# Kernel optimization log

Hardware: AMD Instinct MI355X
Metric: run time of the kernel (lower is better)

The kernel has to match this reference:

```python
import jax, jax.numpy as jnp
import numpy as np

N, D_IN, D_ATTN = 8192, 48, 8


def setup_inputs() -> dict:
    key = jax.random.key(0)
    ks = jax.random.split(key, 9)
    s = 1.0 / np.sqrt(D_IN)
    return {
        "x": jax.random.normal(ks[0], (N, D_IN), jnp.float32),
        "Kw": jax.random.normal(ks[1], (D_IN, D_ATTN), jnp.float32) * s,
        "Kb": jax.random.normal(ks[2], (D_ATTN,), jnp.float32) * s,
        "Qw": jax.random.normal(ks[3], (D_IN, D_ATTN), jnp.float32) * s,
        "Qb": jax.random.normal(ks[4], (D_ATTN,), jnp.float32) * s,
        "Vw": jax.random.normal(ks[5], (D_IN, D_ATTN), jnp.float32) * s,
        "Vb": jax.random.normal(ks[6], (D_ATTN,), jnp.float32) * s,
        "Zw": jax.random.normal(ks[7], (D_ATTN, D_IN), jnp.float32) * (1.0 / np.sqrt(D_ATTN)),
        "Zb": jax.random.normal(ks[8], (D_IN,), jnp.float32) * (1.0 / np.sqrt(D_ATTN)),
    }


def reference(x, Kw, Kb, Qw, Qb, Vw, Vb, Zw, Zb):
    # Tiny QKV projections: [N,48] -> [N,8]
    Xk = x @ Kw + Kb
    Xq = x @ Qw + Qb
    Xv = x @ Vw + Vb
    # Attention over the batch/row dimension: [N,8]@[8,N] -> [N,N]
    scale = jnp.sqrt(jnp.asarray(D_ATTN, jnp.float32))
    AM = jax.nn.softmax(Xk @ Xq.T / scale, axis=1)  # torch F.softmax 2D default dim=1
    Z = AM @ Xv                                      # [N,8]
    return x + (Z @ Zw + Zb)                         # residual + output proj [N,48]
```

## Files before the change

kernel.cpp:

```cpp
#include <hip/hip_runtime.h>
#include <hip/hip_fp16.h>


#define QVJ_OFF  32768
#define BMAX_OFF 131072
#define PART_OFF 131328

typedef _Float16 hv2 __attribute__((ext_vector_type(2)));
union HVU { unsigned u; hv2 v; };

static __device__ __forceinline__ unsigned pku(float a, float b) {
    auto t = __builtin_amdgcn_cvt_pkrtz(a, b);
    union { decltype(t) x; unsigned u; } c; c.x = t; return c.u;
}
static __device__ __forceinline__ float loF(unsigned u) { HVU t; t.u = u; return (float)t.v.x; }
static __device__ __forceinline__ float hiF(unsigned u) { HVU t; t.u = u; return (float)t.v.y; }

__global__ __launch_bounds__(256) void proj_kernel(
    const float* __restrict__ x,
    const float* __restrict__ Kw, const float* __restrict__ Kb,
    const float* __restrict__ Qw, const float* __restrict__ Qb,
    const float* __restrict__ Vw, const float* __restrict__ Vb,
    unsigned* __restrict__ Xksf16, unsigned* __restrict__ QVJ,
    float* __restrict__ bmax)
{
    __shared__ float xs[32 * 49];
    __shared__ float wAll[3 * 388];
    __shared__ float bs[24];
    __shared__ float outv[32][25];
    const int tid = threadIdx.x;
    const int r0 = blockIdx.x * 32;

    for (int i = tid; i < 1536; i += 256) {
        int r = i / 48, c = i - r * 48;
        xs[r * 49 + c] = x[r0 * 48 + i];
    }
    for (int i = tid; i < 384; i += 256) {
        wAll[i]       = Kw[i];
        wAll[388 + i] = Qw[i];
        wAll[776 + i] = Vw[i];
    }
    if (tid < 8)       bs[tid] = Kb[tid];
    else if (tid < 16) bs[tid] = Qb[tid - 8];
    else if (tid < 24) bs[tid] = Vb[tid - 16];
    __syncthreads();

    const int rl = tid >> 3;
    const int g  = tid & 7;
    const int c0 = 3 * g;
    const float* xr = &xs[rl * 49];
    const float* w0 = &wAll[((c0 + 0) >> 3) * 388 + ((c0 + 0) & 7)];
    const float* w1 = &wAll[((c0 + 1) >> 3) * 388 + ((c0 + 1) & 7)];
    const float* w2 = &wAll[((c0 + 2) >> 3) * 388 + ((c0 + 2) & 7)];
    float a0 = bs[c0], a1 = bs[c0 + 1], a2 = bs[c0 + 2];
    #pragma unroll
    for (int k = 0; k < 48; k++) {
        const float xv = xr[k];
        a0 = fmaf(xv, w0[k * 8], a0);
        a1 = fmaf(xv, w1[k * 8], a1);
        a2 = fmaf(xv, w2[k * 8], a2);
    }
    outv[rl][c0] = a0; outv[rl][c0 + 1] = a1; outv[rl][c0 + 2] = a2;
    __syncthreads();

    for (int i = tid; i < 384; i += 256) {
        const int r = i / 12, f = i - r * 12;
        unsigned val;
        if (f < 8) {
            val = __float_as_uint(outv[r][8 + f]);
        } else {
            const int pp = f - 8;
            val = pku(outv[r][16 + 2 * pp], outv[r][16 + 2 * pp + 1]);
        }
        QVJ[((size_t)blockIdx.x * 32 + r) * 12 + f] = val;
    }
    const float kscale = 0.51008732149f;
    if (tid < 32) {
        uint4 o;
        o.x = pku(outv[tid][0] * kscale, outv[tid][1] * kscale);
        o.y = pku(outv[tid][2] * kscale, outv[tid][3] * kscale);
        o.z = pku(outv[tid][4] * kscale, outv[tid][5] * kscale);
        o.w = pku(outv[tid][6] * kscale, outv[tid][7] * kscale);
        ((uint4*)Xksf16)[r0 + tid] = o;
    }
    if (tid >= 192 && tid < 224) {
        const int r = tid - 192;
        float n2 = 0.f;
        #pragma unroll
        for (int c = 0; c < 8; c++) n2 = fmaf(outv[r][8 + c], outv[r][8 + c], n2);
        #pragma unroll
        for (int off = 16; off > 0; off >>= 1)
            n2 = fmaxf(n2, __shfl_xor(n2, off, 64));
        if (r == 0) bmax[blockIdx.x] = n2;
    }
}

__global__ __launch_bounds__(256) void attn_kernel(
    const unsigned* __restrict__ Xksf16, const unsigned* __restrict__ QVJ,
    const float* __restrict__ bmax,
    float* __restrict__ part, int jpw)
{
    __shared__ float shf[4 * 256 * 9];
    uint4*  slab4 = (uint4*)shf;
    float4* slabf = (float4*)shf;
    float*  redf  = shf;

    const int tid  = threadIdx.x;
    const int lane = tid & 63;
    const int wv   = tid >> 6;
    const int rgrp  = blockIdx.x & 31;
    const int chunk = blockIdx.x >> 5;

    float m = fmaxf(fmaxf(bmax[lane], bmax[64 + lane]),
                    fmaxf(bmax[128 + lane], bmax[192 + lane]));
    #pragma unroll
    for (int off = 32; off > 0; off >>= 1)
        m = fmaxf(m, __shfl_xor(m, off, 64));
    const float qmax2 = m;

    float kf[4][8];
    float sinit[4], l[4], acc[4][8];
    #pragma unroll
    for (int i = 0; i < 4; ++i) {
        const uint4 kv = ((const uint4*)Xksf16)[rgrp * 256 + i * 64 + lane];
        kf[i][0] = loF(kv.x); kf[i][1] = hiF(kv.x);
        kf[i][2] = loF(kv.y); kf[i][3] = hiF(kv.y);
        kf[i][4] = loF(kv.z); kf[i][5] = hiF(kv.z);
        kf[i][6] = loF(kv.w); kf[i][7] = hiF(kv.w);
        float kn2 = 0.f;
        #pragma unroll
        for (int c = 0; c < 8; c++) kn2 = fmaf(kf[i][c], kf[i][c], kn2);
        sinit[i] = -sqrtf(kn2 * qmax2);
        l[i] = 0.f;
        #pragma unroll
        for (int c = 0; c < 8; c++) acc[i][c] = 0.f;
    }

    const uint4* QVJ4 = (const uint4*)QVJ;
    const int nt = jpw >> 6;

    for (int t = 0; t < nt; ++t) {
        for (int i = tid; i < 768; i += 256) {
            const int w = i / 192, rec = i - w * 192;
            slab4[i] = QVJ4[((size_t)(chunk * 4 + w) * jpw + t * 64) * 3 + rec];
        }
        __syncthreads();

        const int wbase = wv * 192;
        #pragma unroll 1
        for (int jj = 0; jj < 32; ++jj) {
            const int b = wbase + jj * 6;
            const float4 qa0 = slabf[b + 0];
            const float4 qa1 = slabf[b + 1];
            const uint4  va  = slab4[b + 2];
            const float4 qb0 = slabf[b + 3];
            const float4 qb1 = slabf[b + 4];
            const uint4  vb  = slab4[b + 5];
            const float vA0 = loF(va.x), vA1 = hiF(va.x), vA2 = loF(va.y), vA3 = hiF(va.y);
            const float vA4 = loF(va.z), vA5 = hiF(va.z), vA6 = loF(va.w), vA7 = hiF(va.w);
            const float vB0 = loF(vb.x), vB1 = hiF(vb.x), vB2 = loF(vb.y), vB3 = hiF(vb.y);
            const float vB4 = loF(vb.z), vB5 = hiF(vb.z), vB6 = loF(vb.w), vB7 = hiF(vb.w);
            #pragma unroll
            for (int i = 0; i < 4; ++i) {
                float sA = sinit[i];
                sA = fmaf(kf[i][0], qa0.x, sA);
                sA = fmaf(kf[i][1], qa0.y, sA);
                sA = fmaf(kf[i][2], qa0.z, sA);
                sA = fmaf(kf[i][3], qa0.w, sA);
                sA = fmaf(kf[i][4], qa1.x, sA);
                sA = fmaf(kf[i][5], qa1.y, sA);
                sA = fmaf(kf[i][6], qa1.z, sA);
                sA = fmaf(kf[i][7], qa1.w, sA);
                float sB = sinit[i];
                sB = fmaf(kf[i][0], qb0.x, sB);
                sB = fmaf(kf[i][1], qb0.y, sB);
                sB = fmaf(kf[i][2], qb0.z, sB);
                sB = fmaf(kf[i][3], qb0.w, sB);
                sB = fmaf(kf[i][4], qb1.x, sB);
                sB = fmaf(kf[i][5], qb1.y, sB);
                sB = fmaf(kf[i][6], qb1.z, sB);
                sB = fmaf(kf[i][7], qb1.w, sB);
                const float pA = __builtin_amdgcn_exp2f(sA);
                const float pB = __builtin_amdgcn_exp2f(sB);
                l[i] += pA + pB;
                acc[i][0] = fmaf(pA, vA0, fmaf(pB, vB0, acc[i][0]));
                acc[i][1] = fmaf(pA, vA1, fmaf(pB, vB1, acc[i][1]));
                acc[i][2] = fmaf(pA, vA2, fmaf(pB, vB2, acc[i][2]));
                acc[i][3] = fmaf(pA, vA3, fmaf(pB, vB3, acc[i][3]));
                acc[i][4] = fmaf(pA, vA4, fmaf(pB, vB4, acc[i][4]));
                acc[i][5] = fmaf(pA, vA5, fmaf(pB, vB5, acc[i][5]));
                acc[i][6] = fmaf(pA, vA6, fmaf(pB, vB6, acc[i][6]));
                acc[i][7] = fmaf(pA, vA7, fmaf(pB, vB7, acc[i][7]));
            }
        }
        __syncthreads();
    }

    #pragma unroll
    for (int i = 0; i < 4; ++i) {
        const int r = i * 64 + lane;
        #pragma unroll
        for (int c = 0; c < 8; c++)
            redf[(wv * 256 + r) * 9 + c] = acc[i][c];
        redf[(wv * 256 + r) * 9 + 8] = l[i];
    }
    __syncthreads();
    for (int e = tid; e < 2304; e += 256) {
        const int r = e / 9, c = e - r * 9;
        const float s = redf[(0 * 256 + r) * 9 + c] + redf[(1 * 256 + r) * 9 + c]
                      + redf[(2 * 256 + r) * 9 + c] + redf[(3 * 256 + r) * 9 + c];
        part[((size_t)chunk * 8192 + rgrp * 256 + r) * 9 + c] = s;
    }
}

__global__ __launch_bounds__(256) void finish_kernel(
    const float* __restrict__ x,
    const float* __restrict__ Zw, const float* __restrict__ Zb,
    const float* __restrict__ part, float* __restrict__ out, int nch)
{
    __shared__ float Zs[32 * 9];
    __shared__ float Zl[32];
    __shared__ float zw_s[384];
    __shared__ float zb_s[48];
    const int tid = threadIdx.x;
    const int r0 = blockIdx.x * 32;

    for (int i = tid; i < 384; i += 256) zw_s[i] = Zw[i];
    if (tid < 48) zb_s[tid] = Zb[tid];

    {
        const int r = tid >> 3, c = tid & 7;
        float a = 0.f, l = 0.f;
        #pragma unroll 4
        for (int ch = 0; ch < nch; ch++) {
            const float* p = part + ((size_t)ch * 8192 + r0 + r) * 9;
            a += p[c];
            if (c == 0) l += p[8];
        }
        if (c == 0) Zl[r] = l;
        __syncthreads();
        Zs[r * 9 + c] = a * (1.0f / Zl[r]);
    }
    __syncthreads();

    for (int e = tid; e < 32 * 48; e += 256) {
        const int r = e / 48, c = e - r * 48;
        float o = x[r0 * 48 + e] + zb_s[c];
        #pragma unroll
        for (int k = 0; k < 8; k++) o = fmaf(Zs[r * 9 + k], zw_s[k * 48 + c], o);
        out[r0 * 48 + e] = o;
    }
}

extern "C" void kernel_launch(void* const* d_in, const int* in_sizes, int n_in,
                              void* d_out, int out_size, void* d_ws, size_t ws_size,
                              hipStream_t stream) {
    const float* x  = (const float*)d_in[0];
    const float* Kw = (const float*)d_in[1];
    const float* Kb = (const float*)d_in[2];
    const float* Qw = (const float*)d_in[3];
    const float* Qb = (const float*)d_in[4];
    const float* Vw = (const float*)d_in[5];
    const float* Vb = (const float*)d_in[6];
    const float* Zw = (const float*)d_in[7];
    const float* Zb = (const float*)d_in[8];
    float* out = (float*)d_out;

    float* ws = (float*)d_ws;
    unsigned* Xksf16 = (unsigned*)ws;
    unsigned* QVJ    = (unsigned*)(ws + QVJ_OFF);
    float* bmax      = ws + BMAX_OFF;
    float* part      = ws + PART_OFF;

    int nch = 32;
    const size_t avail = ws_size / 4;
    while (nch > 1 && (size_t)PART_OFF + (size_t)nch * 8192 * 9 > avail) nch >>= 1;
    const int jpw = 2048 / nch;

    proj_kernel<<<256, 256, 0, stream>>>(x, Kw, Kb, Qw, Qb, Vw, Vb,
                                         Xksf16, QVJ, bmax);
    attn_kernel<<<32 * nch, 256, 0, stream>>>(Xksf16, QVJ, bmax, part, jpw);
    finish_kernel<<<256, 256, 0, stream>>>(x, Zw, Zb, part, out, nch);
}
```

Before: 125.2 us.

## Move attention score and PV products onto fp16 MFMA 32x32x16 instructions

Rewrites the attention kernel so each wavefront computes 32x32 score tiles with an fp16 MFMA. The per-row max offset is folded in as an extra K column, and the exponentiated probabilities are fed to two more MFMAs against a transposed V that carries a ones row for the softmax denominator. The projection kernel now emits separate Q, transposed V and key-norm buffers, and the LDS staging and cross-wave reduction are removed. The aim is to replace scalar FMA and exp work with matrix-core throughput, at the cost of fp16 rounding on Q and on the probabilities.

New measurement: 111.3 us. -11.1%, faster.

```diff
diff --git a/kernel.cpp b/kernel.cpp
--- a/kernel.cpp
+++ b/kernel.cpp
@@ -2,26 +2,29 @@
 #include <hip/hip_fp16.h>
 
 
-#define QVJ_OFF  32768
-#define BMAX_OFF 131072
-#define PART_OFF 131328
-
-typedef _Float16 hv2 __attribute__((ext_vector_type(2)));
-union HVU { unsigned u; hv2 v; };
+#define XKS_OFF  0
+#define Q4_OFF   32768
+#define VT_OFF   65536
+#define KN2_OFF  102400
+#define BMAX_OFF 110592
+#define PART_OFF 110848
+
+typedef _Float16 half8 __attribute__((ext_vector_type(8)));
+typedef float f32x16 __attribute__((ext_vector_type(16)));
+union U8 { unsigned u[4]; half8 h; };
 
 static __device__ __forceinline__ unsigned pku(float a, float b) {
     auto t = __builtin_amdgcn_cvt_pkrtz(a, b);
     union { decltype(t) x; unsigned u; } c; c.x = t; return c.u;
 }
-static __device__ __forceinline__ float loF(unsigned u) { HVU t; t.u = u; return (float)t.v.x; }
-static __device__ __forceinline__ float hiF(unsigned u) { HVU t; t.u = u; return (float)t.v.y; }
 
 __global__ __launch_bounds__(256) void proj_kernel(
     const float* __restrict__ x,
     const float* __restrict__ Kw, const float* __restrict__ Kb,
     const float* __restrict__ Qw, const float* __restrict__ Qb,
     const float* __restrict__ Vw, const float* __restrict__ Vb,
-    unsigned* __restrict__ Xksf16, unsigned* __restrict__ QVJ,
+    unsigned* __restrict__ Xksf16, unsigned* __restrict__ Q4,
+    unsigned* __restrict__ Vt, float* __restrict__ kn2,
     float* __restrict__ bmax)
 {
     __shared__ float xs[32 * 49];
@@ -63,17 +66,6 @@
     outv[rl][c0] = a0; outv[rl][c0 + 1] = a1; outv[rl][c0 + 2] = a2;
     __syncthreads();
 
-    for (int i = tid; i < 384; i += 256) {
-        const int r = i / 12, f = i - r * 12;
-        unsigned val;
-        if (f < 8) {
-            val = __float_as_uint(outv[r][8 + f]);
-        } else {
-            const int pp = f - 8;
-            val = pku(outv[r][16 + 2 * pp], outv[r][16 + 2 * pp + 1]);
-        }
-        QVJ[((size_t)blockIdx.x * 32 + r) * 12 + f] = val;
-    }
     const float kscale = 0.51008732149f;
     if (tid < 32) {
         uint4 o;
@@ -82,8 +74,20 @@
         o.z = pku(outv[tid][4] * kscale, outv[tid][5] * kscale);
         o.w = pku(outv[tid][6] * kscale, outv[tid][7] * kscale);
         ((uint4*)Xksf16)[r0 + tid] = o;
-    }
-    if (tid >= 192 && tid < 224) {
+    } else if (tid < 64) {
+        const int r = tid - 32;
+        uint4 o;
+        o.x = pku(outv[r][8],  outv[r][9]);
+        o.y = pku(outv[r][10], outv[r][11]);
+        o.z = pku(outv[r][12], outv[r][13]);
+        o.w = pku(outv[r][14], outv[r][15]);
+        ((uint4*)Q4)[r0 + r] = o;
+    } else if (tid < 192) {
+        const int i = tid - 64;
+        const int c = i >> 4, t = i & 15;
+        Vt[c * 4096 + blockIdx.x * 16 + t] =
+            pku(outv[2 * t][16 + c], outv[2 * t + 1][16 + c]);
+    } else if (tid < 224) {
         const int r = tid - 192;
         float n2 = 0.f;
         #pragma unroll
@@ -92,24 +96,30 @@
         for (int off = 16; off > 0; off >>= 1)
             n2 = fmaxf(n2, __shfl_xor(n2, off, 64));
         if (r == 0) bmax[blockIdx.x] = n2;
-    }
+    } else {
+        const int r = tid - 224;
+        float s = 0.f;
+        #pragma unroll
+        for (int c = 0; c < 8; c++) { const float v = outv[r][c]; s = fmaf(v, v, s); }
+        kn2[r0 + r] = s * (kscale * kscale);
+    }
+    if (tid < 16)
+        Vt[8 * 4096 + blockIdx.x * 16 + tid] = 0x3C003C00u;
 }
 
 __global__ __launch_bounds__(256) void attn_kernel(
-    const unsigned* __restrict__ Xksf16, const unsigned* __restrict__ QVJ,
-    const float* __restrict__ bmax,
-    float* __restrict__ part, int jpw)
+    const uint4* __restrict__ Xks4, const uint4* __restrict__ Q4,
+    const unsigned* __restrict__ Vt, const float* __restrict__ kn2,
+    const float* __restrict__ bmax, float* __restrict__ part, int ntiles)
 {
-    __shared__ float shf[4 * 256 * 9];
-    uint4*  slab4 = (uint4*)shf;
-    float4* slabf = (float4*)shf;
-    float*  redf  = shf;
-
     const int tid  = threadIdx.x;
     const int lane = tid & 63;
     const int wv   = tid >> 6;
-    const int rgrp  = blockIdx.x & 31;
-    const int chunk = blockIdx.x >> 5;
+    const int wid  = blockIdx.x * 4 + wv;
+    const int rg = wid & 255, ch = wid >> 8;
+    const int h = lane >> 5, hl = lane & 31;
+    const int rbase = rg * 32;
+    const int j0base = ch * (ntiles * 32);
 
     float m = fmaxf(fmaxf(bmax[lane], bmax[64 + lane]),
                     fmaxf(bmax[128 + lane], bmax[192 + lane]));
@@ -118,98 +128,67 @@
         m = fmaxf(m, __shfl_xor(m, off, 64));
     const float qmax2 = m;
 
-    float kf[4][8];
-    float sinit[4], l[4], acc[4][8];
-    #pragma unroll
-    for (int i = 0; i < 4; ++i) {
-        const uint4 kv = ((const uint4*)Xksf16)[rgrp * 256 + i * 64 + lane];
-        kf[i][0] = loF(kv.x); kf[i][1] = hiF(kv.x);
-        kf[i][2] = loF(kv.y); kf[i][3] = hiF(kv.y);
-        kf[i][4] = loF(kv.z); kf[i][5] = hiF(kv.z);
-        kf[i][6] = loF(kv.w); kf[i][7] = hiF(kv.w);
-        float kn2 = 0.f;
-        #pragma unroll
-        for (int c = 0; c < 8; c++) kn2 = fmaf(kf[i][c], kf[i][c], kn2);
-        sinit[i] = -sqrtf(kn2 * qmax2);
-        l[i] = 0.f;
-        #pragma unroll
-        for (int c = 0; c < 8; c++) acc[i][c] = 0.f;
-    }
-
-    const uint4* QVJ4 = (const uint4*)QVJ;
-    const int nt = jpw >> 6;
-
-    for (int t = 0; t < nt; ++t) {
-        for (int i = tid; i < 768; i += 256) {
-            const int w = i / 192, rec = i - w * 192;
-            slab4[i] = QVJ4[((size_t)(chunk * 4 + w) * jpw + t * 64) * 3 + rec];
+    U8 Bk;
+    if (h == 0) {
+        const uint4 kv = Xks4[rbase + hl];
+        Bk.u[0] = kv.x; Bk.u[1] = kv.y; Bk.u[2] = kv.z; Bk.u[3] = kv.w;
+    } else {
+        const float sinit = -sqrtf(kn2[rbase + hl] * qmax2);
+        Bk.u[0] = pku(sinit, 0.f); Bk.u[1] = 0u; Bk.u[2] = 0u; Bk.u[3] = 0u;
+    }
+
+    const f32x16 zc = {0.f,0.f,0.f,0.f,0.f,0.f,0.f,0.f,
+                       0.f,0.f,0.f,0.f,0.f,0.f,0.f,0.f};
+    f32x16 acc = {0.f,0.f,0.f,0.f,0.f,0.f,0.f,0.f,
+                  0.f,0.f,0.f,0.f,0.f,0.f,0.f,0.f};
+
+    const int cva = hl;
+    const bool vv = (cva < 9);
+    const uint2* V2 = (const uint2*)Vt;
+
+    for (int t = 0; t < ntiles; ++t) {
+        const int j0 = j0base + t * 32;
+
+        U8 Aq;
+        if (h == 0) {
+            const uint4 qv = Q4[j0 + hl];
+            Aq.u[0] = qv.x; Aq.u[1] = qv.y; Aq.u[2] = qv.z; Aq.u[3] = qv.w;
+        } else {
+            Aq.u[0] = 0x00003C00u; Aq.u[1] = 0u; Aq.u[2] = 0u; Aq.u[3] = 0u;
         }
-        __syncthreads();
-
-        const int wbase = wv * 192;
-        #pragma unroll 1
-        for (int jj = 0; jj < 32; ++jj) {
-            const int b = wbase + jj * 6;
-            const float4 qa0 = slabf[b + 0];
-            const float4 qa1 = slabf[b + 1];
-            const uint4  va  = slab4[b + 2];
-            const float4 qb0 = slabf[b + 3];
-            const float4 qb1 = slabf[b + 4];
-            const uint4  vb  = slab4[b + 5];
-            const float vA0 = loF(va.x), vA1 = hiF(va.x), vA2 = loF(va.y), vA3 = hiF(va.y);
-            const float vA4 = loF(va.z), vA5 = hiF(va.z), vA6 = loF(va.w), vA7 = hiF(va.w);
-            const float vB0 = loF(vb.x), vB1 = hiF(vb.x), vB2 = loF(vb.y), vB3 = hiF(vb.y);
-            const float vB4 = loF(vb.z), vB5 = hiF(vb.z), vB6 = loF(vb.w), vB7 = hiF(vb.w);
-            #pragma unroll
-            for (int i = 0; i < 4; ++i) {
-                float sA = sinit[i];
-                sA = fmaf(kf[i][0], qa0.x, sA);
-                sA = fmaf(kf[i][1], qa0.y, sA);
-                sA = fmaf(kf[i][2], qa0.z, sA);
-                sA = fmaf(kf[i][3], qa0.w, sA);
-                sA = fmaf(kf[i][4], qa1.x, sA);
-                sA = fmaf(kf[i][5], qa1.y, sA);
-                sA = fmaf(kf[i][6], qa1.z, sA);
-                sA = fmaf(kf[i][7], qa1.w, sA);
-                float sB = sinit[i];
-                sB = fmaf(kf[i][0], qb0.x, sB);
-                sB = fmaf(kf[i][1], qb0.y, sB);
-                sB = fmaf(kf[i][2], qb0.z, sB);
-                sB = fmaf(kf[i][3], qb0.w, sB);
-                sB = fmaf(kf[i][4], qb1.x, sB);
-                sB = fmaf(kf[i][5], qb1.y, sB);
-                sB = fmaf(kf[i][6], qb1.z, sB);
-                sB = fmaf(kf[i][7], qb1.w, sB);
-                const float pA = __builtin_amdgcn_exp2f(sA);
-                const float pB = __builtin_amdgcn_exp2f(sB);
-                l[i] += pA + pB;
-                acc[i][0] = fmaf(pA, vA0, fmaf(pB, vB0, acc[i][0]));
-                acc[i][1] = fmaf(pA, vA1, fmaf(pB, vB1, acc[i][1]));
-                acc[i][2] = fmaf(pA, vA2, fmaf(pB, vB2, acc[i][2]));
-                acc[i][3] = fmaf(pA, vA3, fmaf(pB, vB3, acc[i][3]));
-                acc[i][4] = fmaf(pA, vA4, fmaf(pB, vB4, acc[i][4]));
-                acc[i][5] = fmaf(pA, vA5, fmaf(pB, vB5, acc[i][5]));
-                acc[i][6] = fmaf(pA, vA6, fmaf(pB, vB6, acc[i][6]));
-                acc[i][7] = fmaf(pA, vA7, fmaf(pB, vB7, acc[i][7]));
-            }
+        const f32x16 s = __builtin_amdgcn_mfma_f32_32x32x16_f16(Aq.h, Bk.h, zc, 0, 0, 0);
+
+        const unsigned pk01 = pku(__builtin_amdgcn_exp2f(s[0]),  __builtin_amdgcn_exp2f(s[1]));
+        const unsigned pk23 = pku(__builtin_amdgcn_exp2f(s[2]),  __builtin_amdgcn_exp2f(s[3]));
+        const unsigned pk45 = pku(__builtin_amdgcn_exp2f(s[4]),  __builtin_amdgcn_exp2f(s[5]));
+        const unsigned pk67 = pku(__builtin_amdgcn_exp2f(s[6]),  __builtin_amdgcn_exp2f(s[7]));
+        const unsigned pk89 = pku(__builtin_amdgcn_exp2f(s[8]),  __builtin_amdgcn_exp2f(s[9]));
+        const unsigned pkAB = pku(__builtin_amdgcn_exp2f(s[10]), __builtin_amdgcn_exp2f(s[11]));
+        const unsigned pkCD = pku(__builtin_amdgcn_exp2f(s[12]), __builtin_amdgcn_exp2f(s[13]));
+        const unsigned pkEF = pku(__builtin_amdgcn_exp2f(s[14]), __builtin_amdgcn_exp2f(s[15]));
+
+        uint2 va0 = {0u,0u}, va1 = {0u,0u}, va2 = {0u,0u}, va3 = {0u,0u};
+        if (vv) {
+            const int vb = cva * 8192 + j0 + 4 * h;
+            va0 = V2[(vb)      >> 2];
+            va1 = V2[(vb + 8)  >> 2];
+            va2 = V2[(vb + 16) >> 2];
+            va3 = V2[(vb + 24) >> 2];
         }
-        __syncthreads();
-    }
-
-    #pragma unroll
-    for (int i = 0; i < 4; ++i) {
-        const int r = i * 64 + lane;
-        #pragma unroll
-        for (int c = 0; c < 8; c++)
-            redf[(wv * 256 + r) * 9 + c] = acc[i][c];
-        redf[(wv * 256 + r) * 9 + 8] = l[i];
-    }
-    __syncthreads();
-    for (int e = tid; e < 2304; e += 256) {
-        const int r = e / 9, c = e - r * 9;
-        const float s = redf[(0 * 256 + r) * 9 + c] + redf[(1 * 256 + r) * 9 + c]
-                      + redf[(2 * 256 + r) * 9 + c] + redf[(3 * 256 + r) * 9 + c];
-        part[((size_t)chunk * 8192 + rgrp * 256 + r) * 9 + c] = s;
+        U8 A2a; A2a.u[0] = va0.x; A2a.u[1] = va0.y; A2a.u[2] = va1.x; A2a.u[3] = va1.y;
+        U8 B2a; B2a.u[0] = pk01;  B2a.u[1] = pk23;  B2a.u[2] = pk45;  B2a.u[3] = pk67;
+        acc = __builtin_amdgcn_mfma_f32_32x32x16_f16(A2a.h, B2a.h, acc, 0, 0, 0);
+        U8 A2b; A2b.u[0] = va2.x; A2b.u[1] = va2.y; A2b.u[2] = va3.x; A2b.u[3] = va3.y;
+        U8 B2b; B2b.u[0] = pk89;  B2b.u[1] = pkAB;  B2b.u[2] = pkCD;  B2b.u[3] = pkEF;
+        acc = __builtin_amdgcn_mfma_f32_32x32x16_f16(A2b.h, B2b.h, acc, 0, 0, 0);
+    }
+
+    float* pr = part + ((size_t)ch * 8192 + rbase + hl) * 9;
+    if (h == 0) {
+        pr[0] = acc[0]; pr[1] = acc[1]; pr[2] = acc[2]; pr[3] = acc[3];
+        pr[8] = acc[4];
+    } else {
+        pr[4] = acc[0]; pr[5] = acc[1]; pr[6] = acc[2]; pr[7] = acc[3];
     }
 }
 
@@ -267,18 +246,22 @@
     float* out = (float*)d_out;
 
     float* ws = (float*)d_ws;
-    unsigned* Xksf16 = (unsigned*)ws;
-    unsigned* QVJ    = (unsigned*)(ws + QVJ_OFF);
+    unsigned* Xksf16 = (unsigned*)(ws + XKS_OFF);
+    unsigned* Q4     = (unsigned*)(ws + Q4_OFF);
+    unsigned* Vt     = (unsigned*)(ws + VT_OFF);
+    float* kn2       = ws + KN2_OFF;
     float* bmax      = ws + BMAX_OFF;
     float* part      = ws + PART_OFF;
 
     int nch = 32;
     const size_t avail = ws_size / 4;
     while (nch > 1 && (size_t)PART_OFF + (size_t)nch * 8192 * 9 > avail) nch >>= 1;
-    const int jpw = 2048 / nch;
+    const int ntiles = 256 / nch;
 
     proj_kernel<<<256, 256, 0, stream>>>(x, Kw, Kb, Qw, Qb, Vw, Vb,
-                                         Xksf16, QVJ, bmax);
-    attn_kernel<<<32 * nch, 256, 0, stream>>>(Xksf16, QVJ, bmax, part, jpw);
+                                         Xksf16, Q4, Vt, kn2, bmax);
+    attn_kernel<<<64 * nch, 256, 0, stream>>>((const uint4*)Xksf16,
+                                              (const uint4*)Q4, Vt, kn2,
+                                              bmax, part, ntiles);
     finish_kernel<<<256, 256, 0, stream>>>(x, Zw, Zb, part, out, nch);
 }
```
